# Performance work log

Hardware: AMD Instinct MI355X
Metric: run time of the kernel (lower is better)

Reference implementation:

```python
import jax, jax.numpy as jnp
import numpy as np

B, C, F = 4096, 64, 128  # batch, num_channels (nodes), embedding_dim == hidden_dim
L = 3                    # num_layers


def setup_inputs() -> dict:
    key = jax.random.key(0)
    ks = jax.random.split(key, 2 * L + 3)
    s = 1.0 / np.sqrt(F)
    inp = {"embeddings": jax.random.normal(ks[0], (B, C, F), dtype=jnp.float32)}
    for l in range(L):
        inp[f"W{l}"] = jax.random.normal(ks[1 + 2 * l], (F, F), dtype=jnp.float32) * s
        inp[f"b{l}"] = jnp.zeros((F,), dtype=jnp.float32)
    inp["Wr"] = jax.random.normal(ks[2 * L + 1], (F, F), dtype=jnp.float32) * s
    inp["br"] = jnp.zeros((F,), dtype=jnp.float32)
    return inp


def reference(embeddings, W0, b0, W1, b1, W2, b2, Wr, br):
    # edge_index = all ordered pairs of distinct nodes (complete graph).
    # GCNConv adds self-loops and normalizes by D^{-1/2}(A+I)D^{-1/2};
    # on a complete graph every degree is C, so A_hat[i,j] = 1/C for all i,j.
    C_nodes = embeddings.shape[1]
    A_hat = jnp.full((C_nodes, C_nodes), 1.0 / C_nodes, dtype=embeddings.dtype)

    x = embeddings  # [B, C, F] — batch loop in the original is vectorized here
    for W, b in ((W0, b0), (W1, b1), (W2, b2)):
        xw = jnp.einsum("bcf,fh->bch", x, W)          # node-wise transform
        x = jax.nn.relu(jnp.einsum("cn,bnh->bch", A_hat, xw) + b)  # aggregate
    pooled = x.mean(axis=1)                            # [B, F] mean readout
    return pooled @ Wr + br                            # [B, F]
```

## Files before the change

kernel.cpp:

```cpp
#include <hip/hip_runtime.h>

#define B_ 4096
#define C_ 64
#define F_ 128
#define KP 136
#define GRP 16
#define NBLK (B_ / GRP)
#define WSLICE 8192
#define WLAYER 32768

typedef __attribute__((ext_vector_type(8))) short short8;
typedef __attribute__((ext_vector_type(4))) float f32x4;

__device__ __forceinline__ unsigned short bf16_trunc(float f) {
    union { float f; unsigned u; } v; v.f = f;
    return (unsigned short)(v.u >> 16);
}
__device__ __forceinline__ float bf16_tof(unsigned short h) {
    union { unsigned u; float f; } v; v.u = ((unsigned)h) << 16;
    return v.f;
}

__global__ __launch_bounds__(256) void mean_prep_kernel(const float* __restrict__ emb,
                                                        float* __restrict__ ebar,
                                                        const float* __restrict__ W0,
                                                        const float* __restrict__ W1,
                                                        const float* __restrict__ W2,
                                                        const float* __restrict__ Wr,
                                                        unsigned short* __restrict__ wprep) {
    __shared__ float4 part[8][32];
    __shared__ float  tile[128 * 17];

    const int b = blockIdx.x;
    const int t = threadIdx.x;
    const int fc = t & 31;
    const int cr = t >> 5;

    {
        const float4* src = (const float4*)(emb + (size_t)b * C_ * F_);
        float4 s = make_float4(0.f, 0.f, 0.f, 0.f);
        #pragma unroll
        for (int c = 0; c < C_ / 8; ++c) {
            float4 v = src[(cr + c * 8) * (F_ / 4) + fc];
            s.x += v.x; s.y += v.y; s.z += v.z; s.w += v.w;
        }
        part[cr][fc] = s;
        __syncthreads();
        if (t < 32) {
            float4 acc = part[0][t];
            #pragma unroll
            for (int i = 1; i < 8; ++i) {
                float4 v = part[i][t];
                acc.x += v.x; acc.y += v.y; acc.z += v.z; acc.w += v.w;
            }
            const float inv = 1.0f / (float)C_;
            acc.x *= inv; acc.y *= inv; acc.z *= inv; acc.w *= inv;
            ((float4*)(ebar + (size_t)b * F_))[t] = acc;
        }
    }

    if (b < 32) {
        const int layer = b >> 3;
        const int s     = b & 7;
        const float* W = layer == 0 ? W0 : layer == 1 ? W1 : layer == 2 ? W2 : Wr;

        {
            const int kk = t & 127, half = t >> 7;
            const float4* wr_ = (const float4*)(W + (size_t)kk * F_ + 16 * s + 8 * half);
            const float4 v0 = wr_[0], v1 = wr_[1];
            float* dst = tile + kk * 17 + 8 * half;
            dst[0] = v0.x; dst[1] = v0.y; dst[2] = v0.z; dst[3] = v0.w;
            dst[4] = v1.x; dst[5] = v1.y; dst[6] = v1.z; dst[7] = v1.w;
        }
        __syncthreads();
        {
            const int ln = t & 63;
            const int c = ln & 15, q = ln >> 4;
            const int kkpl_base = t >> 6;
            #pragma unroll
            for (int rep = 0; rep < 2; ++rep) {
                const int kkpl = kkpl_base + rep * 4;
                const int kk = kkpl >> 1, pl = kkpl & 1;
                unsigned wd[4];
                #pragma unroll
                for (int p = 0; p < 4; ++p) {
                    unsigned short u[2];
                    #pragma unroll
                    for (int h2 = 0; h2 < 2; ++h2) {
                        const int e = 2 * p + h2;
                        const float f = tile[(kk * 32 + q * 8 + e) * 17 + c];
                        const unsigned short hi = bf16_trunc(f);
                        u[h2] = (pl == 0) ? hi : bf16_trunc(f - bf16_tof(hi));
                    }
                    wd[p] = (unsigned)u[0] | ((unsigned)u[1] << 16);
                }
                const size_t dst = ((size_t)(layer * 4 + (s >> 1)) * 16
                                    + (size_t)((s & 1) * 8 + kkpl)) * 512 + ln * 8;
                *(int4*)(wprep + dst) = make_int4(wd[0], wd[1], wd[2], wd[3]);
            }
        }
    }
}

__global__ __launch_bounds__(512, 2) void mlp_mfma_kernel(
    const float* __restrict__ ebar,
    const unsigned short* __restrict__ wprep,
    const float* __restrict__ b0, const float* __restrict__ b1,
    const float* __restrict__ b2, const float* __restrict__ br,
    float* __restrict__ out)
{
    __shared__ unsigned short xb[2][2 * GRP * KP];

    const int t    = threadIdx.x;
    const int row0 = blockIdx.x * GRP;
    const int w = t >> 6, l = t & 63;
    const int q = l >> 4, c = l & 15;

    const unsigned short* wbase = wprep + (size_t)(w >> 1) * WSLICE
                                        + (size_t)(w & 1) * 8 * 512;

    short8 wA[8], wB[8];
    #pragma unroll
    for (int f = 0; f < 8; ++f)
        wA[f] = *(const short8*)&wbase[(size_t)f * 512 + l * 8];

    {
        const float4* src = (const float4*)(ebar + (size_t)row0 * F_);
        const int idx = t;
        const int r = idx >> 5, c4 = idx & 31;
        const float4 v = src[idx];
        ushort4 h, lo;
        h.x = bf16_trunc(v.x); lo.x = bf16_trunc(v.x - bf16_tof(h.x));
        h.y = bf16_trunc(v.y); lo.y = bf16_trunc(v.y - bf16_tof(h.y));
        h.z = bf16_trunc(v.z); lo.z = bf16_trunc(v.z - bf16_tof(h.z));
        h.w = bf16_trunc(v.w); lo.w = bf16_trunc(v.w - bf16_tof(h.w));
        *(ushort4*)&xb[0][(0 * GRP + r) * KP + c4 * 4] = h;
        *(ushort4*)&xb[0][(1 * GRP + r) * KP + c4 * 4] = lo;
    }
    __syncthreads();

    const float* bs[4] = {b0, b1, b2, br};
    float biasr[4];
    #pragma unroll
    for (int L = 0; L < 4; ++L) biasr[L] = bs[L][w * 16 + c];

    auto layer_body = [&](int L, short8 (&CUR)[8], short8 (&NXT)[8],
                          const unsigned short* xcur, unsigned short* xnxt) {
        if (L < 3) {
            const unsigned short* nb = wbase + (size_t)(L + 1) * WLAYER;
            #pragma unroll
            for (int f = 0; f < 8; ++f)
                NXT[f] = *(const short8*)&nb[(size_t)f * 512 + l * 8];
        }

        f32x4 acc = (f32x4){0.f, 0.f, 0.f, 0.f};

        #pragma unroll
        for (int kk = 0; kk < 4; ++kk) {
            const int ko = kk * 32 + q * 8;
            const short8 ah = *(const short8*)&xcur[(0 * GRP + c) * KP + ko];
            const short8 al = *(const short8*)&xcur[(1 * GRP + c) * KP + ko];
            const short8 bh = CUR[kk * 2 + 0];
            const short8 bl = CUR[kk * 2 + 1];
            acc = __builtin_amdgcn_mfma_f32_16x16x32_bf16(ah, bh, acc, 0, 0, 0);
            acc = __builtin_amdgcn_mfma_f32_16x16x32_bf16(al, bh, acc, 0, 0, 0);
            acc = __builtin_amdgcn_mfma_f32_16x16x32_bf16(ah, bl, acc, 0, 0, 0);
        }

        if (L < 3) {
            #pragma unroll
            for (int j = 0; j < 4; ++j) {
                float v = acc[j] + biasr[L];
                v = fmaxf(v, 0.f);
                const int row = q * 4 + j;
                const int col = w * 16 + c;
                const unsigned short h = bf16_trunc(v);
                xnxt[(0 * GRP + row) * KP + col] = h;
                xnxt[(1 * GRP + row) * KP + col] = bf16_trunc(v - bf16_tof(h));
            }
            __syncthreads();
        } else {
            #pragma unroll
            for (int j = 0; j < 4; ++j)
                out[(size_t)(row0 + q * 4 + j) * F_ + w * 16 + c]
                    = acc[j] + biasr[3];
        }
    };

    layer_body(0, wA, wB, xb[0], xb[1]);
    layer_body(1, wB, wA, xb[1], xb[0]);
    layer_body(2, wA, wB, xb[0], xb[1]);
    layer_body(3, wB, wA, xb[1], nullptr);
}

extern "C" void kernel_launch(void* const* d_in, const int* in_sizes, int n_in,
                              void* d_out, int out_size, void* d_ws, size_t ws_size,
                              hipStream_t stream) {
    const float* emb = (const float*)d_in[0];
    const float* W0  = (const float*)d_in[1];
    const float* b0  = (const float*)d_in[2];
    const float* W1  = (const float*)d_in[3];
    const float* b1  = (const float*)d_in[4];
    const float* W2  = (const float*)d_in[5];
    const float* b2  = (const float*)d_in[6];
    const float* Wr  = (const float*)d_in[7];
    const float* br  = (const float*)d_in[8];

    float*          ebar  = (float*)d_ws;
    unsigned short* wprep = (unsigned short*)((char*)d_ws + 2097152);

    mean_prep_kernel<<<B_, 256, 0, stream>>>(emb, ebar, W0, W1, W2, Wr, wprep);
    mlp_mfma_kernel<<<NBLK, 512, 0, stream>>>(ebar, wprep, b0, b1, b2, br,
                                              (float*)d_out);
}
```

Before: 29.37 us.

## Restructure channel-mean reduction to per-thread streaming and emit bf16 hi/lo splits

The mean-reduction kernel drops from one 256-thread block per batch row (8-way split plus a shared-memory reduction) to 512 blocks in which each thread sums all 64 channels for one float4 column, using two accumulators. There is no longer any shared-memory reduction or barrier for the mean. The bf16 hi/lo split of the mean moves from the MLP kernel into the prep kernel, so the MLP kernel loads ready-made bf16 pairs. The aim is fewer blocks and syncs and more memory-level parallelism on the 128 MB streaming read, at the cost of longer per-thread dependency chains and strided reads that rely on cross-thread coalescing.

```diff
diff --git a/kernel.cpp b/kernel.cpp
--- a/kernel.cpp
+++ b/kernel.cpp
@@ -21,47 +21,21 @@
     return v.f;
 }
 
-__global__ __launch_bounds__(256) void mean_prep_kernel(const float* __restrict__ emb,
-                                                        float* __restrict__ ebar,
-                                                        const float* __restrict__ W0,
-                                                        const float* __restrict__ W1,
-                                                        const float* __restrict__ W2,
-                                                        const float* __restrict__ Wr,
-                                                        unsigned short* __restrict__ wprep) {
-    __shared__ float4 part[8][32];
-    __shared__ float  tile[128 * 17];
-
-    const int b = blockIdx.x;
-    const int t = threadIdx.x;
-    const int fc = t & 31;
-    const int cr = t >> 5;
-
-    {
-        const float4* src = (const float4*)(emb + (size_t)b * C_ * F_);
-        float4 s = make_float4(0.f, 0.f, 0.f, 0.f);
-        #pragma unroll
-        for (int c = 0; c < C_ / 8; ++c) {
-            float4 v = src[(cr + c * 8) * (F_ / 4) + fc];
-            s.x += v.x; s.y += v.y; s.z += v.z; s.w += v.w;
-        }
-        part[cr][fc] = s;
-        __syncthreads();
-        if (t < 32) {
-            float4 acc = part[0][t];
-            #pragma unroll
-            for (int i = 1; i < 8; ++i) {
-                float4 v = part[i][t];
-                acc.x += v.x; acc.y += v.y; acc.z += v.z; acc.w += v.w;
-            }
-            const float inv = 1.0f / (float)C_;
-            acc.x *= inv; acc.y *= inv; acc.z *= inv; acc.w *= inv;
-            ((float4*)(ebar + (size_t)b * F_))[t] = acc;
-        }
-    }
-
-    if (b < 32) {
-        const int layer = b >> 3;
-        const int s     = b & 7;
+__global__ __launch_bounds__(256) void stream_prep_kernel(
+    const float* __restrict__ emb,
+    unsigned short* __restrict__ ebh, unsigned short* __restrict__ ebl,
+    const float* __restrict__ W0, const float* __restrict__ W1,
+    const float* __restrict__ W2, const float* __restrict__ Wr,
+    unsigned short* __restrict__ wprep)
+{
+    __shared__ float tile[128 * 17];
+
+    const int t   = threadIdx.x;
+    const int blk = blockIdx.x;
+
+    if (blk < 32) {
+        const int layer = blk >> 3;
+        const int s     = blk & 7;
         const float* W = layer == 0 ? W0 : layer == 1 ? W1 : layer == 2 ? W2 : Wr;
 
         {
@@ -99,11 +73,38 @@
                 *(int4*)(wprep + dst) = make_int4(wd[0], wd[1], wd[2], wd[3]);
             }
         }
+        __syncthreads();
     }
+
+    const int idx = blk * 256 + t;
+    const int b   = idx >> 5, f4 = idx & 31;
+    const float4* src = (const float4*)(emb + (size_t)b * C_ * F_) + f4;
+
+    float4 aA = make_float4(0.f, 0.f, 0.f, 0.f);
+    float4 aB = make_float4(0.f, 0.f, 0.f, 0.f);
+    #pragma unroll 8
+    for (int c = 0; c < 32; ++c) {
+        const float4 v0 = src[(2 * c)     * 32];
+        const float4 v1 = src[(2 * c + 1) * 32];
+        aA.x += v0.x; aA.y += v0.y; aA.z += v0.z; aA.w += v0.w;
+        aB.x += v1.x; aB.y += v1.y; aB.z += v1.z; aB.w += v1.w;
+    }
+    const float inv = 1.0f / (float)C_;
+    float m[4];
+    m[0] = (aA.x + aB.x) * inv; m[1] = (aA.y + aB.y) * inv;
+    m[2] = (aA.z + aB.z) * inv; m[3] = (aA.w + aB.w) * inv;
+
+    ushort4 h, lo;
+    h.x = bf16_trunc(m[0]); lo.x = bf16_trunc(m[0] - bf16_tof(h.x));
+    h.y = bf16_trunc(m[1]); lo.y = bf16_trunc(m[1] - bf16_tof(h.y));
+    h.z = bf16_trunc(m[2]); lo.z = bf16_trunc(m[2] - bf16_tof(h.z));
+    h.w = bf16_trunc(m[3]); lo.w = bf16_trunc(m[3] - bf16_tof(h.w));
+    *(ushort4*)&ebh[(size_t)b * F_ + f4 * 4] = h;
+    *(ushort4*)&ebl[(size_t)b * F_ + f4 * 4] = lo;
 }
 
 __global__ __launch_bounds__(512, 2) void mlp_mfma_kernel(
-    const float* __restrict__ ebar,
+    const unsigned short* __restrict__ ebh, const unsigned short* __restrict__ ebl,
     const unsigned short* __restrict__ wprep,
     const float* __restrict__ b0, const float* __restrict__ b1,
     const float* __restrict__ b2, const float* __restrict__ br,
@@ -125,15 +126,9 @@
         wA[f] = *(const short8*)&wbase[(size_t)f * 512 + l * 8];
 
     {
-        const float4* src = (const float4*)(ebar + (size_t)row0 * F_);
-        const int idx = t;
-        const int r = idx >> 5, c4 = idx & 31;
-        const float4 v = src[idx];
-        ushort4 h, lo;
-        h.x = bf16_trunc(v.x); lo.x = bf16_trunc(v.x - bf16_tof(h.x));
-        h.y = bf16_trunc(v.y); lo.y = bf16_trunc(v.y - bf16_tof(h.y));
-        h.z = bf16_trunc(v.z); lo.z = bf16_trunc(v.z - bf16_tof(h.z));
-        h.w = bf16_trunc(v.w); lo.w = bf16_trunc(v.w - bf16_tof(h.w));
+        const int r = t >> 5, c4 = t & 31;
+        const ushort4 h  = *(const ushort4*)&ebh[(size_t)(row0 + r) * F_ + c4 * 4];
+        const ushort4 lo = *(const ushort4*)&ebl[(size_t)(row0 + r) * F_ + c4 * 4];
         *(ushort4*)&xb[0][(0 * GRP + r) * KP + c4 * 4] = h;
         *(ushort4*)&xb[0][(1 * GRP + r) * KP + c4 * 4] = lo;
     }
@@ -206,10 +201,13 @@
     const float* Wr  = (const float*)d_in[7];
     const float* br  = (const float*)d_in[8];
 
-    float*          ebar  = (float*)d_ws;
-    unsigned short* wprep = (unsigned short*)((char*)d_ws + 2097152);
-
-    mean_prep_kernel<<<B_, 256, 0, stream>>>(emb, ebar, W0, W1, W2, Wr, wprep);
-    mlp_mfma_kernel<<<NBLK, 512, 0, stream>>>(ebar, wprep, b0, b1, b2, br,
-                                              (float*)d_out);
-}
+    char* ws = (char*)d_ws;
+    unsigned short* ebh   = (unsigned short*)ws;
+    unsigned short* ebl   = (unsigned short*)(ws + 1048576);
+    unsigned short* wprep = (unsigned short*)(ws + 2097152);
+
+    stream_prep_kernel<<<512, 256, 0, stream>>>(emb, ebh, ebl,
+                                                W0, W1, W2, Wr, wprep);
+    mlp_mfma_kernel<<<NBLK, 512, 0, stream>>>(ebh, ebl, wprep,
+                                              b0, b1, b2, br, (float*)d_out);
+}
```

Result: slower. 34.10 us (+16.1%).
